# Optimization experiments

Hardware: AMD Instinct MI355X
Metric: run time of the kernel (lower is better)

The kernel has to match this reference:

```python
import jax, jax.numpy as jnp
import numpy as np

CURV = 0.9            # geoopt PoincareBall(0.9)
SQRT_C = CURV ** 0.5
MIN_NORM = 1e-15
PROJ_EPS = 4e-3       # geoopt float32 boundary eps
ATANH_EPS = 1e-7
COS_EPS = 1e-8        # torch.cosine_similarity eps


def _norm(x):
    return jnp.sqrt(jnp.maximum(jnp.sum(x * x, axis=-1, keepdims=True), MIN_NORM * MIN_NORM))


def _project(x):
    # project onto ball of radius (1-eps)/sqrt(c)
    n = jnp.maximum(_norm(x), MIN_NORM)
    maxnorm = (1.0 - PROJ_EPS) / SQRT_C
    return jnp.where(n > maxnorm, x / n * maxnorm, x)


def expmap0(u):
    n = jnp.maximum(_norm(u), MIN_NORM)
    gamma = jnp.tanh(SQRT_C * n) * u / (SQRT_C * n)
    return _project(gamma)


def mobius_add(x, y):
    c = CURV
    x2 = jnp.sum(x * x, axis=-1, keepdims=True)
    y2 = jnp.sum(y * y, axis=-1, keepdims=True)
    xy = jnp.sum(x * y, axis=-1, keepdims=True)
    num = (1.0 + 2.0 * c * xy + c * y2) * x + (1.0 - c * x2) * y
    den = 1.0 + 2.0 * c * xy + c * c * x2 * y2
    return num / jnp.maximum(den, MIN_NORM)


def pdist(x, y):
    # dist(x,y) = 2/sqrt(c) * artanh(sqrt(c) * ||(-x) (+) y||)
    d = mobius_add(-x, y)
    n = _norm(d)[..., 0]
    z = jnp.clip(SQRT_C * n, -1.0 + ATANH_EPS, 1.0 - ATANH_EPS)
    return 2.0 / SQRT_C * jnp.arctanh(z)


def cos_sim(a, b):
    na = jnp.maximum(jnp.sqrt(jnp.sum(a * a, axis=-1)), COS_EPS)
    nb = jnp.maximum(jnp.sqrt(jnp.sum(b * b, axis=-1)), COS_EPS)
    return jnp.sum(a * b, axis=-1) / (na * nb)


def setup_inputs() -> dict:
    key = jax.random.key(0)
    ks = jax.random.split(key, 11)
    B, L, Ls, C, Lc, H, R = 4, 512, 128, 20, 128, 768, 512
    s = 0.02  # keep projected embeddings in a realistic range
    return {
        "text_out": jax.random.normal(ks[0], (B, L, H), jnp.float32),
        "summary_out": jax.random.normal(ks[1], (B, Ls, H), jnp.float32),
        "candidate_out": jax.random.normal(ks[2], (B, C, Lc, H), jnp.float32),
        "W_d": jax.random.normal(ks[3], (H, R), jnp.float32) * s,
        "W_s": jax.random.normal(ks[4], (H, R), jnp.float32) * s,
        "W_c": jax.random.normal(ks[5], (H, R), jnp.float32) * s,
        "W_p": jax.random.normal(ks[6], (R, R), jnp.float32) * s,
        "conv_w1": jax.random.normal(ks[7], (1, H, R), jnp.float32) * s,
        "conv_b1": jax.random.normal(ks[8], (R,), jnp.float32) * s,
        "conv_w2": jax.random.normal(ks[9], (2, H, R), jnp.float32) * s,
        "conv_b2": jax.random.normal(ks[10], (R,), jnp.float32) * s,
    }


def _forward(text_out, summary_out, candidate_out, W_d, W_s, W_c, W_p,
             conv_w1, conv_b1, conv_w2, conv_b2):
    # --- document ---
    doc_emb = expmap0(text_out[:, 0, :] @ W_d)                       # [B,R]

    # NGramers (max_gram=2, eval mode so dropout is identity)
    x = text_out[:, 1:-1, :]                                         # [B,L-2,H]
    y1 = jax.nn.relu(jnp.einsum('blh,hr->blr', x, conv_w1[0]) + conv_b1)
    y2 = jax.nn.relu(jnp.einsum('blh,hr->blr', x[:, :-1], conv_w2[0])
                     + jnp.einsum('blh,hr->blr', x[:, 1:], conv_w2[1]) + conv_b2)
    gram = jnp.concatenate([y1, y2], axis=1)                         # [B,2L-5,R]

    doc_word_emb = expmap0(jnp.einsum('blr,rk->blk', gram, W_p))     # [B,T,R]
    doc_inter = 1.0 / pdist(doc_word_emb, doc_emb[:, None, :])       # [B,T]

    # --- summary ---
    summary_emb = expmap0(jnp.max(summary_out, axis=1) @ W_s)        # [B,R]
    summary_score = -pdist(summary_emb, doc_emb) ** 2                # [B]
    sum_inter = 1.0 / pdist(doc_word_emb, summary_emb[:, None, :])   # [B,T]
    summary_score = summary_score + cos_sim(doc_inter, sum_inter)    # [B]

    # --- candidates ---
    cand_emb = expmap0(jnp.einsum('bch,hr->bcr', jnp.max(candidate_out, axis=2), W_c))  # [B,C,R]
    score = -pdist(cand_emb, doc_emb[:, None, :]) ** 2               # [B,C]
    cand_inter = 1.0 / pdist(doc_word_emb[:, None, :, :], cand_emb[:, :, None, :])      # [B,C,T]
    score = score + cos_sim(doc_inter[:, None, :], cand_inter)       # [B,C]
    return score, summary_score


def reference(text_out, summary_out, candidate_out, W_d, W_s, W_c, W_p,
              conv_w1, conv_b1, conv_w2, conv_b2):
    return _forward(text_out, summary_out, candidate_out, W_d, W_s, W_c, W_p,
                    conv_w1, conv_b1, conv_w2, conv_b2)
```

## Files before the change

### kernel.cpp

```cpp
#include <hip/hip_runtime.h>
#include <math.h>

#define SQRTC  0.94868329805051381f
#define MAXN   (0.996f/SQRTC)
#define OME_CLIP (1.0f - 0.996f*0.996f)
#define TWO_OVER_SQRTC 2.1081851067789197f

typedef unsigned short u16;
typedef __attribute__((ext_vector_type(8))) short bf8;
typedef __attribute__((ext_vector_type(4))) float f4;

__device__ __forceinline__ u16 f2bf(float f){
    union { float f; unsigned int i; } v; v.f = f;
    unsigned int x = v.i;
    unsigned int lsb = (x >> 16) & 1u;
    x += 0x7fffu + lsb;
    return (u16)(x >> 16);
}
__device__ __forceinline__ float bf2f(u16 u){
    union { unsigned int i; float f; } v; v.i = ((unsigned int)u) << 16; return v.f;
}

__device__ __forceinline__ void gload16(void* lds, const void* g){
    __builtin_amdgcn_global_load_lds(
        (const __attribute__((address_space(1))) unsigned int*)g,
        (__attribute__((address_space(3))) unsigned int*)lds,
        16, 0, 0);
}

__device__ __forceinline__ float pdist_stable(float ome_x, float ome_y, float t){
    float u = 1.0f - ome_x, v = 1.0f - ome_y;
    float den = fmaxf(1.0f - 1.8f*t + u*v, 1e-15f);
    float q = ome_x*ome_y/den;
    q = fminf(fmaxf(q, 2.0e-7f), 1.0f);
    float z = sqrtf(fmaxf(1.0f - q, 0.0f));
    float at = 0.5f * logf((1.0f+z)*(1.0f+z)/q);
    return TWO_OVER_SQRTC * at;
}

__device__ __forceinline__ void expmap_scale_ome(float sum, float* fout, float* omeout){
    float nraw = sqrtf(fmaxf(sum, 1e-30f));
    float n = fmaxf(nraw, 1e-15f);
    float sn = SQRTC*n;
    float th = tanhf(sn);
    float factor = th/sn;
    float gn = factor*nraw;
    if (gn > MAXN){ *fout = factor*(MAXN/gn); *omeout = OME_CLIP; }
    else { *fout = factor; *omeout = fmaxf((1.0f-th)*(1.0f+th), 1e-12f); }
}

__global__ __launch_bounds__(256)
void k_stage1(const float* __restrict__ summ, const float* __restrict__ cand,
              const float* __restrict__ text,
              const float* __restrict__ w1, const float* __restrict__ w2,
              const float* __restrict__ wp,
              float* __restrict__ smax, float* __restrict__ cmax,
              u16* __restrict__ textb, u16* __restrict__ w1t,
              u16* __restrict__ w2t, u16* __restrict__ wpt)
{
    __shared__ float shm[1056];
    int bx = blockIdx.x;
    int t = threadIdx.x;
    if (bx < 252){
        int row = bx / 3, hc = bx - row*3;
        int w = t >> 6, lane = t & 63;
        const float* in = (row < 4) ? (summ + (long long)row*128*768)
                                    : (cand + (long long)(row-4)*128*768);
        const float* p = in + (long long)(w*32)*768 + hc*256 + lane*4;
        float4 m = make_float4(-INFINITY,-INFINITY,-INFINITY,-INFINITY);
        #pragma unroll 8
        for (int l = 0; l < 32; l++){
            float4 v = *(const float4*)(p + (long long)l*768);
            m.x = fmaxf(m.x, v.x); m.y = fmaxf(m.y, v.y);
            m.z = fmaxf(m.z, v.z); m.w = fmaxf(m.w, v.w);
        }
        float4* sm4 = (float4*)shm;
        sm4[w*64 + lane] = m; __syncthreads();
        if (t < 64){
            float4 a = sm4[t], b4 = sm4[64+t], c4 = sm4[128+t], d4 = sm4[192+t];
            float4 r;
            r.x = fmaxf(fmaxf(a.x,b4.x), fmaxf(c4.x,d4.x));
            r.y = fmaxf(fmaxf(a.y,b4.y), fmaxf(c4.y,d4.y));
            r.z = fmaxf(fmaxf(a.z,b4.z), fmaxf(c4.z,d4.z));
            r.w = fmaxf(fmaxf(a.w,b4.w), fmaxf(c4.w,d4.w));
            float* outp = (row < 4) ? (smax + row*768) : (cmax + (row-4)*768);
            *(float4*)(outp + hc*256 + t*4) = r;
        }
        return;
    }
    int pb = bx - 252;
    if (pb < 768){
        int base = pb*2048 + t*8;
        float4 a = *(const float4*)(text + base);
        float4 b = *(const float4*)(text + base + 4);
        *(ushort4*)(textb + base)     = make_ushort4(f2bf(a.x), f2bf(a.y), f2bf(a.z), f2bf(a.w));
        *(ushort4*)(textb + base + 4) = make_ushort4(f2bf(b.x), f2bf(b.y), f2bf(b.z), f2bf(b.w));
        return;
    }
    int j = pb - 768;
    const float* in; u16* outp; int K;
    if (j < 384){ in = w1; outp = w1t; K = 768; }
    else if (j < 1152){ j -= 384; in = w2; outp = w2t; K = 1536; }
    else { j -= 1152; in = wp; outp = wpt; K = 512; }
    const int N = 512, ntile = N/32;
    int k0 = (j/ntile)*32, n0 = (j - (j/ntile)*ntile)*32;
    int tx = t & 31, ty = t >> 5;
    #pragma unroll
    for (int i = 0; i < 4; i++)
        shm[(ty*4+i)*33 + tx] = in[(long long)(k0 + ty*4 + i)*N + n0 + tx];
    __syncthreads();
    #pragma unroll
    for (int i = 0; i < 4; i++)
        outp[(long long)(n0 + ty*4 + i)*K + k0 + tx] = f2bf(shm[tx*33 + ty*4+i]);
}

__global__ __launch_bounds__(256)
void k_stage2(const u16* __restrict__ textb,
              const u16* __restrict__ w1t, const u16* __restrict__ w2t,
              const float* __restrict__ cb1, const float* __restrict__ cb2,
              const float* __restrict__ text,
              const float* __restrict__ smax, const float* __restrict__ cmax,
              const float* __restrict__ W_d, const float* __restrict__ W_s,
              const float* __restrict__ W_c,
              u16* __restrict__ gram, float* __restrict__ emb_all)
{
    __shared__ char smem[16384];
    int bx = blockIdx.x;
    int t = threadIdx.x;
    if (bx < 512){
        u16* As = (u16*)smem;
        u16* Bs = (u16*)(smem + 8192);
        int xx = bx & 63, yy = bx >> 6;
        int job = xx & 1;
        int m0 = (xx >> 1) * 64;
        int n0 = yy * 64;
        int K   = job ? 1536 : 768;
        int M   = job ? 2036 : 2040;
        int rpb = job ? 509 : 510;
        int ob  = job ? 510 : 0;
        const u16* Bt = job ? w2t : w1t;
        const float* bias = job ? cb2 : cb1;

        int r0 = t >> 3;
        int co = (((t & 7) ^ (r0 & 7)) << 3);

        int gm0 = m0 + r0;      if (gm0 >= M) gm0 = M - 1;
        int gm1 = m0 + r0 + 32; if (gm1 >= M) gm1 = M - 1;
        int ab0 = gm0 / rpb, al0 = gm0 - ab0*rpb;
        int ab1 = gm1 / rpb, al1 = gm1 - ab1*rpb;
        const u16* a0 = textb + (long long)ab0*393216 + (long long)(al0+1)*768 + co;
        const u16* a1 = textb + (long long)ab1*393216 + (long long)(al1+1)*768 + co;
        const u16* bp0 = Bt + (long long)(n0 + r0)*K      + co;
        const u16* bp1 = Bt + (long long)(n0 + r0 + 32)*K + co;
        u16* lA0 = As + t*8;
        u16* lA1 = As + (256 + t)*8;
        u16* lB0 = Bs + t*8;
        u16* lB1 = Bs + (256 + t)*8;

        int lane = t & 63, wv = t >> 6;
        int fm = lane & 15, fq = lane >> 4;
        int arow = wv*16 + fm;
        int aswz = arow & 7, bswz = fm & 7;
        int aoff0 = arow*64 + ((fq     ^ aswz) << 3);
        int aoff1 = arow*64 + (((4+fq) ^ aswz) << 3);
        int boff0 = ((fq     ^ bswz) << 3);
        int boff1 = (((4+fq) ^ bswz) << 3);

        f4 acc0 = {0,0,0,0}, acc1 = {0,0,0,0}, acc2 = {0,0,0,0}, acc3 = {0,0,0,0};
        for (int k0 = 0; k0 < K; k0 += 64){
            gload16(lA0, a0 + k0);
            gload16(lA1, a1 + k0);
            gload16(lB0, bp0 + k0);
            gload16(lB1, bp1 + k0);
            __syncthreads();
            bf8 af0 = *(const bf8*)(As + aoff0);
            bf8 af1 = *(const bf8*)(As + aoff1);
            bf8 b00 = *(const bf8*)(Bs + (fm   )*64 + boff0);
            bf8 b10 = *(const bf8*)(Bs + (16+fm)*64 + boff0);
            bf8 b20 = *(const bf8*)(Bs + (32+fm)*64 + boff0);
            bf8 b30 = *(const bf8*)(Bs + (48+fm)*64 + boff0);
            bf8 b01 = *(const bf8*)(Bs + (fm   )*64 + boff1);
            bf8 b11 = *(const bf8*)(Bs + (16+fm)*64 + boff1);
            bf8 b21 = *(const bf8*)(Bs + (32+fm)*64 + boff1);
            bf8 b31 = *(const bf8*)(Bs + (48+fm)*64 + boff1);
            acc0 = __builtin_amdgcn_mfma_f32_16x16x32_bf16(af0, b00, acc0, 0, 0, 0);
            acc1 = __builtin_amdgcn_mfma_f32_16x16x32_bf16(af0, b10, acc1, 0, 0, 0);
            acc2 = __builtin_amdgcn_mfma_f32_16x16x32_bf16(af0, b20, acc2, 0, 0, 0);
            acc3 = __builtin_amdgcn_mfma_f32_16x16x32_bf16(af0, b30, acc3, 0, 0, 0);
            acc0 = __builtin_amdgcn_mfma_f32_16x16x32_bf16(af1, b01, acc0, 0, 0, 0);
            acc1 = __builtin_amdgcn_mfma_f32_16x16x32_bf16(af1, b11, acc1, 0, 0, 0);
            acc2 = __builtin_amdgcn_mfma_f32_16x16x32_bf16(af1, b21, acc2, 0, 0, 0);
            acc3 = __builtin_amdgcn_mfma_f32_16x16x32_bf16(af1, b31, acc3, 0, 0, 0);
            __syncthreads();
        }
        int col = n0 + fm;
        float bv0 = bias[col], bv1 = bias[col+16], bv2 = bias[col+32], bv3 = bias[col+48];
        #pragma unroll
        for (int i = 0; i < 4; i++){
            int row = m0 + wv*16 + fq*4 + i;
            if (row >= M) continue;
            int b = row/rpb, l = row - b*rpb;
            long long orow = (long long)b*1019 + ob + l;
            u16* gp = gram + orow*512;
            gp[col]      = f2bf(fmaxf(acc0[i] + bv0, 0.f));
            gp[col + 16] = f2bf(fmaxf(acc1[i] + bv1, 0.f));
            gp[col + 32] = f2bf(fmaxf(acc2[i] + bv2, 0.f));
            gp[col + 48] = f2bf(fmaxf(acc3[i] + bv3, 0.f));
        }
        return;
    }
    {
        int eb = bx - 512;
        int row = eb >> 3, nt = eb & 7;
        float* a   = (float*)smem;
        float* red = (float*)smem + 768;
        const float* A; const float* W;
        if (row < 4){ A = text + (long long)row*512*768; W = W_d; }
        else if (row < 8){ A = smax + (long long)(row-4)*768; W = W_s; }
        else { A = cmax + (long long)(row-8)*768; W = W_c; }
        for (int k = t; k < 768; k += 256) a[k] = A[k];
        __syncthreads();
        int lane = t & 63, kg = t >> 6;
        int col = nt*64 + lane;
        const float* Wp = W + (long long)(kg*192)*512 + col;
        float acc = 0.f;
        #pragma unroll 8
        for (int k = 0; k < 192; k++) acc += a[kg*192 + k] * Wp[k*512];
        red[t] = acc; __syncthreads();
        if (t < 64) emb_all[(long long)row*512 + col] = red[t] + red[t+64] + red[t+128] + red[t+192];
    }
}

__global__ __launch_bounds__(256)
void k_stage3(const u16* __restrict__ gram, const u16* __restrict__ wpt,
              u16* __restrict__ dwe_b,
              float* __restrict__ emb_all, float* __restrict__ ome_all,
              u16* __restrict__ emb_b)
{
    __shared__ char smem[16384];
    int bx = blockIdx.x;
    int t = threadIdx.x;
    if (bx < 512){
        u16* As = (u16*)smem;
        u16* Bs = (u16*)(smem + 8192);
        const int K = 512, M = 4076;
        int m0 = (bx >> 3) * 64;
        int n0 = (bx & 7) * 64;

        int r0 = t >> 3;
        int co = (((t & 7) ^ (r0 & 7)) << 3);
        int gm0 = m0 + r0;      if (gm0 >= M) gm0 = M - 1;
        int gm1 = m0 + r0 + 32; if (gm1 >= M) gm1 = M - 1;
        const u16* a0 = gram + (long long)gm0*512 + co;
        const u16* a1 = gram + (long long)gm1*512 + co;
        const u16* bp0 = wpt + (long long)(n0 + r0)*K      + co;
        const u16* bp1 = wpt + (long long)(n0 + r0 + 32)*K + co;
        u16* lA0 = As + t*8;
        u16* lA1 = As + (256 + t)*8;
        u16* lB0 = Bs + t*8;
        u16* lB1 = Bs + (256 + t)*8;

        int lane = t & 63, wv = t >> 6;
        int fm = lane & 15, fq = lane >> 4;
        int arow = wv*16 + fm;
        int aswz = arow & 7, bswz = fm & 7;
        int aoff0 = arow*64 + ((fq     ^ aswz) << 3);
        int aoff1 = arow*64 + (((4+fq) ^ aswz) << 3);
        int boff0 = ((fq     ^ bswz) << 3);
        int boff1 = (((4+fq) ^ bswz) << 3);

        f4 acc0 = {0,0,0,0}, acc1 = {0,0,0,0}, acc2 = {0,0,0,0}, acc3 = {0,0,0,0};
        for (int k0 = 0; k0 < K; k0 += 64){
            gload16(lA0, a0 + k0);
            gload16(lA1, a1 + k0);
            gload16(lB0, bp0 + k0);
            gload16(lB1, bp1 + k0);
            __syncthreads();
            bf8 af0 = *(const bf8*)(As + aoff0);
            bf8 af1 = *(const bf8*)(As + aoff1);
            bf8 b00 = *(const bf8*)(Bs + (fm   )*64 + boff0);
            bf8 b10 = *(const bf8*)(Bs + (16+fm)*64 + boff0);
            bf8 b20 = *(const bf8*)(Bs + (32+fm)*64 + boff0);
            bf8 b30 = *(const bf8*)(Bs + (48+fm)*64 + boff0);
            bf8 b01 = *(const bf8*)(Bs + (fm   )*64 + boff1);
            bf8 b11 = *(const bf8*)(Bs + (16+fm)*64 + boff1);
            bf8 b21 = *(const bf8*)(Bs + (32+fm)*64 + boff1);
            bf8 b31 = *(const bf8*)(Bs + (48+fm)*64 + boff1);
            acc0 = __builtin_amdgcn_mfma_f32_16x16x32_bf16(af0, b00, acc0, 0, 0, 0);
            acc1 = __builtin_amdgcn_mfma_f32_16x16x32_bf16(af0, b10, acc1, 0, 0, 0);
            acc2 = __builtin_amdgcn_mfma_f32_16x16x32_bf16(af0, b20, acc2, 0, 0, 0);
            acc3 = __builtin_amdgcn_mfma_f32_16x16x32_bf16(af0, b30, acc3, 0, 0, 0);
            acc0 = __builtin_amdgcn_mfma_f32_16x16x32_bf16(af1, b01, acc0, 0, 0, 0);
            acc1 = __builtin_amdgcn_mfma_f32_16x16x32_bf16(af1, b11, acc1, 0, 0, 0);
            acc2 = __builtin_amdgcn_mfma_f32_16x16x32_bf16(af1, b21, acc2, 0, 0, 0);
            acc3 = __builtin_amdgcn_mfma_f32_16x16x32_bf16(af1, b31, acc3, 0, 0, 0);
            __syncthreads();
        }
        int col = n0 + fm;
        #pragma unroll
        for (int i = 0; i < 4; i++){
            int row = m0 + wv*16 + fq*4 + i;
            if (row >= M) continue;
            u16* dp = dwe_b + (long long)row*512;
            dp[col]      = f2bf(acc0[i]);
            dp[col + 16] = f2bf(acc1[i]);
            dp[col + 32] = f2bf(acc2[i]);
            dp[col + 48] = f2bf(acc3[i]);
        }
        return;
    }
    {
        float* red = (float*)smem;
        int row = bx - 512;
        float* X = emb_all + (long long)row*512;
        float2 u = *(float2*)(X + t*2);
        red[t] = u.x*u.x + u.y*u.y; __syncthreads();
        for (int s = 128; s > 0; s >>= 1){ if (t < s) red[t] += red[t+s]; __syncthreads(); }
        float f, ome;
        expmap_scale_ome(red[0], &f, &ome);
        float sx = u.x*f, sy = u.y*f;
        *(float2*)(X + t*2) = make_float2(sx, sy);
        u16* Xb = emb_b + (long long)row*512;
        Xb[t*2]   = f2bf(sx);
        Xb[t*2+1] = f2bf(sy);
        if (t == 0) ome_all[row] = ome;
    }
}

__global__ __launch_bounds__(64)
void k_dots_mfma(const u16* __restrict__ dwe_b, const u16* __restrict__ emb_b,
                 const float* __restrict__ ome_all,
                 float* __restrict__ doc_inter, float* __restrict__ sum_inter,
                 float* __restrict__ cand_inter)
{
    int bx = blockIdx.x;
    int b  = bx >> 6;
    int m0 = (bx & 63) * 16;
    int t = threadIdx.x;
    int fm = t & 15, fq = t >> 4;

    int arow = m0 + fm; if (arow > 1018) arow = 1018;
    const u16* Ap = dwe_b + ((long long)(b*1019 + arow))*512 + fq*8;

    int n1 = 16 + fm; if (n1 > 21) n1 = 21;
    int e0 = (fm == 0) ? b : (fm == 1) ? 4 + b : 8 + b*20 + (fm - 2);
    int e1 = 8 + b*20 + (n1 - 2);
    const u16* B0 = emb_b + (long long)e0*512 + fq*8;
    const u16* B1 = emb_b + (long long)e1*512 + fq*8;
    float oy0 = ome_all[e0];
    float oy1 = ome_all[e1];

    f4 acc0 = {0,0,0,0}, acc1 = {0,0,0,0};
    float ssq = 0.f;
    #pragma unroll 4
    for (int k0 = 0; k0 < 512; k0 += 32){
        bf8 av  = *(const bf8*)(Ap + k0);
        bf8 bv0 = *(const bf8*)(B0 + k0);
        bf8 bv1 = *(const bf8*)(B1 + k0);
        #pragma unroll
        for (int j = 0; j < 8; j++){ float x = bf2f(((u16*)&av)[j]); ssq += x*x; }
        acc0 = __builtin_amdgcn_mfma_f32_16x16x32_bf16(av, bv0, acc0, 0, 0, 0);
        acc1 = __builtin_amdgcn_mfma_f32_16x16x32_bf16(av, bv1, acc1, 0, 0, 0);
    }
    ssq += __shfl_xor(ssq, 16);
    ssq += __shfl_xor(ssq, 32);

    #pragma unroll
    for (int i = 0; i < 4; i++){
        int r = fq*4 + i;
        float rs = __shfl(ssq, r);
        int row = m0 + r;
        if (row >= 1019) continue;
        float f, ox;
        expmap_scale_ome(rs, &f, &ox);
        long long grow = (long long)b*1019 + row;
        {
            float s = acc0[i] * f;
            float dist = pdist_stable(ox, oy0, s);
            float inv = 1.0f/fmaxf(dist, 1e-12f);
            if (fm == 0) doc_inter[grow] = inv;
            else if (fm == 1) sum_inter[grow] = inv;
            else cand_inter[((long long)(b*20 + (fm - 2)))*1019 + row] = inv;
        }
        if (16 + fm < 22){
            float s = acc1[i] * f;
            float dist = pdist_stable(ox, oy1, s);
            float inv = 1.0f/fmaxf(dist, 1e-12f);
            cand_inter[((long long)(b*20 + (16 + fm - 2)))*1019 + row] = inv;
        }
    }
}

__global__ __launch_bounds__(256)
void k_final(const float* __restrict__ doc_inter, const float* __restrict__ sum_inter,
             const float* __restrict__ cand_inter,
             const float* __restrict__ emb_all, const float* __restrict__ ome_all,
             float* __restrict__ out)
{
    __shared__ float r0[256], r1[256], r2[256], r3[256];
    int j = blockIdx.x, t = threadIdx.x;
    int b; const float *a, *bb; int xi, yi; int outIdx;
    if (j < 80){
        b = j/20;
        a  = doc_inter + b*1019;
        bb = cand_inter + (long long)j*1019;
        xi = 8 + j; yi = b;
        outIdx = j;
    } else {
        b = j - 80;
        a  = doc_inter + b*1019;
        bb = sum_inter + b*1019;
        xi = 4 + b; yi = b;
        outIdx = 80 + b;
    }
    const float* xe = emb_all + (long long)xi*512;
    const float* ye = emb_all + (long long)yi*512;
    float ox = ome_all[xi], oy = ome_all[yi];
    float saa = 0.f, sbb = 0.f, sab = 0.f, st = 0.f;
    for (int l = t; l < 1019; l += 256){ float av = a[l], bv = bb[l]; saa += av*av; sbb += bv*bv; sab += av*bv; }
    for (int k = t; k < 512; k += 256) st += xe[k]*ye[k];
    r0[t] = saa; r1[t] = sbb; r2[t] = sab; r3[t] = st; __syncthreads();
    for (int s = 128; s > 0; s >>= 1){
        if (t < s){ r0[t] += r0[t+s]; r1[t] += r1[t+s]; r2[t] += r2[t+s]; r3[t] += r3[t+s]; }
        __syncthreads();
    }
    if (t == 0){
        float na = fmaxf(sqrtf(r0[0]), 1e-8f);
        float nb = fmaxf(sqrtf(r1[0]), 1e-8f);
        float cosv = r2[0] / (na*nb);
        float pd = pdist_stable(ox, oy, r3[0]);
        out[outIdx] = -pd*pd + cosv;
    }
}

extern "C" void kernel_launch(void* const* d_in, const int* in_sizes, int n_in,
                              void* d_out, int out_size, void* d_ws, size_t ws_size,
                              hipStream_t stream) {
    const float* text = (const float*)d_in[0];
    const float* summ = (const float*)d_in[1];
    const float* cand = (const float*)d_in[2];
    const float* W_d  = (const float*)d_in[3];
    const float* W_s  = (const float*)d_in[4];
    const float* W_c  = (const float*)d_in[5];
    const float* W_p  = (const float*)d_in[6];
    const float* cw1  = (const float*)d_in[7];
    const float* cb1  = (const float*)d_in[8];
    const float* cw2  = (const float*)d_in[9];
    const float* cb2  = (const float*)d_in[10];
    float* out = (float*)d_out;

    const int B = 4, C = 20, H = 768;

    char* base = (char*)d_ws;
    size_t off = 0;
    auto allocF = [&](size_t n)->float*{ float* p = (float*)(base + off); off += ((n*4) + 255) & ~(size_t)255; return p; };
    auto allocU = [&](size_t n)->u16*{ u16* p = (u16*)(base + off); off += ((n*2) + 255) & ~(size_t)255; return p; };

    float* smax = allocF(B*H);
    float* cmax = allocF(B*C*H);
    float* emb_all = allocF(88*512);
    float* ome_all = allocF(88);
    u16* emb_b = allocU(88*512);
    u16* textb = allocU(4*512*768);
    u16* w1t   = allocU(512*768);
    u16* w2t   = allocU(512*1536);
    u16* wpt   = allocU(512*512);
    u16* gram  = allocU(4076*512);
    u16* dwe_b = allocU(4076*512);
    float* doc_inter = allocF(4076);
    float* sum_inter = allocF(4076);
    float* cand_inter= allocF(B*C*1019);

    k_stage1<<<2428, 256, 0, stream>>>(summ, cand, text, cw1, cw2, W_p,
                                       smax, cmax, textb, w1t, w2t, wpt);

    k_stage2<<<1216, 256, 0, stream>>>(textb, w1t, w2t, cb1, cb2,
                                       text, smax, cmax, W_d, W_s, W_c,
                                       gram, emb_all);

    k_stage3<<<600, 256, 0, stream>>>(gram, wpt, dwe_b, emb_all, ome_all, emb_b);

    k_dots_mfma<<<256, 64, 0, stream>>>(dwe_b, emb_b, ome_all,
                                        doc_inter, sum_inter, cand_inter);

    k_final<<<84, 256, 0, stream>>>(doc_inter, sum_inter, cand_inter,
                                    emb_all, ome_all, out);
}
```

Measured before the change: 141.4 us.

## Double-buffer LDS tiles in stage2 and stage3 GEMMs to overlap loads with MFMA

Both bf16 MFMA GEMM paths now use two LDS buffers for A and B. The global-to-LDS loads for the next K tile are issued before computing the current one, with explicit vmcnt waits and raw s_barrier in place of __syncthreads. The aim is to hide global load latency behind the MFMA work. The cost is doubled shared memory per block, which may reduce occupancy. Correctness now depends on the hand-written waitcnt and barrier ordering.

```diff
diff --git a/kernel.cpp b/kernel.cpp
--- a/kernel.cpp
+++ b/kernel.cpp
@@ -124,12 +124,14 @@
               const float* __restrict__ W_c,
               u16* __restrict__ gram, float* __restrict__ emb_all)
 {
-    __shared__ char smem[16384];
+    __shared__ char smem[32768];
     int bx = blockIdx.x;
     int t = threadIdx.x;
     if (bx < 512){
-        u16* As = (u16*)smem;
-        u16* Bs = (u16*)(smem + 8192);
+        u16* As0 = (u16*)smem;
+        u16* Bs0 = (u16*)(smem + 8192);
+        u16* As1 = (u16*)(smem + 16384);
+        u16* Bs1 = (u16*)(smem + 24576);
         int xx = bx & 63, yy = bx >> 6;
         int job = xx & 1;
         int m0 = (xx >> 1) * 64;
@@ -152,10 +154,7 @@
         const u16* a1 = textb + (long long)ab1*393216 + (long long)(al1+1)*768 + co;
         const u16* bp0 = Bt + (long long)(n0 + r0)*K      + co;
         const u16* bp1 = Bt + (long long)(n0 + r0 + 32)*K + co;
-        u16* lA0 = As + t*8;
-        u16* lA1 = As + (256 + t)*8;
-        u16* lB0 = Bs + t*8;
-        u16* lB1 = Bs + (256 + t)*8;
+        int d0 = t*8, d1 = (256 + t)*8;
 
         int lane = t & 63, wv = t >> 6;
         int fm = lane & 15, fq = lane >> 4;
@@ -167,22 +166,37 @@
         int boff1 = (((4+fq) ^ bswz) << 3);
 
         f4 acc0 = {0,0,0,0}, acc1 = {0,0,0,0}, acc2 = {0,0,0,0}, acc3 = {0,0,0,0};
-        for (int k0 = 0; k0 < K; k0 += 64){
-            gload16(lA0, a0 + k0);
-            gload16(lA1, a1 + k0);
-            gload16(lB0, bp0 + k0);
-            gload16(lB1, bp1 + k0);
-            __syncthreads();
-            bf8 af0 = *(const bf8*)(As + aoff0);
-            bf8 af1 = *(const bf8*)(As + aoff1);
-            bf8 b00 = *(const bf8*)(Bs + (fm   )*64 + boff0);
-            bf8 b10 = *(const bf8*)(Bs + (16+fm)*64 + boff0);
-            bf8 b20 = *(const bf8*)(Bs + (32+fm)*64 + boff0);
-            bf8 b30 = *(const bf8*)(Bs + (48+fm)*64 + boff0);
-            bf8 b01 = *(const bf8*)(Bs + (fm   )*64 + boff1);
-            bf8 b11 = *(const bf8*)(Bs + (16+fm)*64 + boff1);
-            bf8 b21 = *(const bf8*)(Bs + (32+fm)*64 + boff1);
-            bf8 b31 = *(const bf8*)(Bs + (48+fm)*64 + boff1);
+        const int nt = K >> 6;
+        gload16(As0 + d0, a0);
+        gload16(As0 + d1, a1);
+        gload16(Bs0 + d0, bp0);
+        gload16(Bs0 + d1, bp1);
+        for (int i = 0; i < nt; i++){
+            u16* Ac = (i & 1) ? As1 : As0;
+            u16* Bc = (i & 1) ? Bs1 : Bs0;
+            if (i + 1 < nt){
+                u16* An = (i & 1) ? As0 : As1;
+                u16* Bn = (i & 1) ? Bs0 : Bs1;
+                int kn = (i + 1) << 6;
+                gload16(An + d0, a0 + kn);
+                gload16(An + d1, a1 + kn);
+                gload16(Bn + d0, bp0 + kn);
+                gload16(Bn + d1, bp1 + kn);
+                asm volatile("s_waitcnt vmcnt(4)" ::: "memory");
+            } else {
+                asm volatile("s_waitcnt vmcnt(0)" ::: "memory");
+            }
+            __builtin_amdgcn_s_barrier();
+            bf8 af0 = *(const bf8*)(Ac + aoff0);
+            bf8 af1 = *(const bf8*)(Ac + aoff1);
+            bf8 b00 = *(const bf8*)(Bc + (fm   )*64 + boff0);
+            bf8 b10 = *(const bf8*)(Bc + (16+fm)*64 + boff0);
+            bf8 b20 = *(const bf8*)(Bc + (32+fm)*64 + boff0);
+            bf8 b30 = *(const bf8*)(Bc + (48+fm)*64 + boff0);
+            bf8 b01 = *(const bf8*)(Bc + (fm   )*64 + boff1);
+            bf8 b11 = *(const bf8*)(Bc + (16+fm)*64 + boff1);
+            bf8 b21 = *(const bf8*)(Bc + (32+fm)*64 + boff1);
+            bf8 b31 = *(const bf8*)(Bc + (48+fm)*64 + boff1);
             acc0 = __builtin_amdgcn_mfma_f32_16x16x32_bf16(af0, b00, acc0, 0, 0, 0);
             acc1 = __builtin_amdgcn_mfma_f32_16x16x32_bf16(af0, b10, acc1, 0, 0, 0);
             acc2 = __builtin_amdgcn_mfma_f32_16x16x32_bf16(af0, b20, acc2, 0, 0, 0);
@@ -191,7 +205,7 @@
             acc1 = __builtin_amdgcn_mfma_f32_16x16x32_bf16(af1, b11, acc1, 0, 0, 0);
             acc2 = __builtin_amdgcn_mfma_f32_16x16x32_bf16(af1, b21, acc2, 0, 0, 0);
             acc3 = __builtin_amdgcn_mfma_f32_16x16x32_bf16(af1, b31, acc3, 0, 0, 0);
-            __syncthreads();
+            __builtin_amdgcn_s_barrier();
         }
         int col = n0 + fm;
         float bv0 = bias[col], bv1 = bias[col+16], bv2 = bias[col+32], bv3 = bias[col+48];
@@ -237,12 +251,14 @@
               float* __restrict__ emb_all, float* __restrict__ ome_all,
               u16* __restrict__ emb_b)
 {
-    __shared__ char smem[16384];
+    __shared__ char smem[32768];
     int bx = blockIdx.x;
     int t = threadIdx.x;
     if (bx < 512){
-        u16* As = (u16*)smem;
-        u16* Bs = (u16*)(smem + 8192);
+        u16* As0 = (u16*)smem;
+        u16* Bs0 = (u16*)(smem + 8192);
+        u16* As1 = (u16*)(smem + 16384);
+        u16* Bs1 = (u16*)(smem + 24576);
         const int K = 512, M = 4076;
         int m0 = (bx >> 3) * 64;
         int n0 = (bx & 7) * 64;
@@ -255,10 +271,7 @@
         const u16* a1 = gram + (long long)gm1*512 + co;
         const u16* bp0 = wpt + (long long)(n0 + r0)*K      + co;
         const u16* bp1 = wpt + (long long)(n0 + r0 + 32)*K + co;
-        u16* lA0 = As + t*8;
-        u16* lA1 = As + (256 + t)*8;
-        u16* lB0 = Bs + t*8;
-        u16* lB1 = Bs + (256 + t)*8;
+        int d0 = t*8, d1 = (256 + t)*8;
 
         int lane = t & 63, wv = t >> 6;
         int fm = lane & 15, fq = lane >> 4;
@@ -270,22 +283,37 @@
         int boff1 = (((4+fq) ^ bswz) << 3);
 
         f4 acc0 = {0,0,0,0}, acc1 = {0,0,0,0}, acc2 = {0,0,0,0}, acc3 = {0,0,0,0};
-        for (int k0 = 0; k0 < K; k0 += 64){
-            gload16(lA0, a0 + k0);
-            gload16(lA1, a1 + k0);
-            gload16(lB0, bp0 + k0);
-            gload16(lB1, bp1 + k0);
-            __syncthreads();
-            bf8 af0 = *(const bf8*)(As + aoff0);
-            bf8 af1 = *(const bf8*)(As + aoff1);
-            bf8 b00 = *(const bf8*)(Bs + (fm   )*64 + boff0);
-            bf8 b10 = *(const bf8*)(Bs + (16+fm)*64 + boff0);
-            bf8 b20 = *(const bf8*)(Bs + (32+fm)*64 + boff0);
-            bf8 b30 = *(const bf8*)(Bs + (48+fm)*64 + boff0);
-            bf8 b01 = *(const bf8*)(Bs + (fm   )*64 + boff1);
-            bf8 b11 = *(const bf8*)(Bs + (16+fm)*64 + boff1);
-            bf8 b21 = *(const bf8*)(Bs + (32+fm)*64 + boff1);
-            bf8 b31 = *(const bf8*)(Bs + (48+fm)*64 + boff1);
+        const int nt = K >> 6;
+        gload16(As0 + d0, a0);
+        gload16(As0 + d1, a1);
+        gload16(Bs0 + d0, bp0);
+        gload16(Bs0 + d1, bp1);
+        for (int i = 0; i < nt; i++){
+            u16* Ac = (i & 1) ? As1 : As0;
+            u16* Bc = (i & 1) ? Bs1 : Bs0;
+            if (i + 1 < nt){
+                u16* An = (i & 1) ? As0 : As1;
+                u16* Bn = (i & 1) ? Bs0 : Bs1;
+                int kn = (i + 1) << 6;
+                gload16(An + d0, a0 + kn);
+                gload16(An + d1, a1 + kn);
+                gload16(Bn + d0, bp0 + kn);
+                gload16(Bn + d1, bp1 + kn);
+                asm volatile("s_waitcnt vmcnt(4)" ::: "memory");
+            } else {
+                asm volatile("s_waitcnt vmcnt(0)" ::: "memory");
+            }
+            __builtin_amdgcn_s_barrier();
+            bf8 af0 = *(const bf8*)(Ac + aoff0);
+            bf8 af1 = *(const bf8*)(Ac + aoff1);
+            bf8 b00 = *(const bf8*)(Bc + (fm   )*64 + boff0);
+            bf8 b10 = *(const bf8*)(Bc + (16+fm)*64 + boff0);
+            bf8 b20 = *(const bf8*)(Bc + (32+fm)*64 + boff0);
+            bf8 b30 = *(const bf8*)(Bc + (48+fm)*64 + boff0);
+            bf8 b01 = *(const bf8*)(Bc + (fm   )*64 + boff1);
+            bf8 b11 = *(const bf8*)(Bc + (16+fm)*64 + boff1);
+            bf8 b21 = *(const bf8*)(Bc + (32+fm)*64 + boff1);
+            bf8 b31 = *(const bf8*)(Bc + (48+fm)*64 + boff1);
             acc0 = __builtin_amdgcn_mfma_f32_16x16x32_bf16(af0, b00, acc0, 0, 0, 0);
             acc1 = __builtin_amdgcn_mfma_f32_16x16x32_bf16(af0, b10, acc1, 0, 0, 0);
             acc2 = __builtin_amdgcn_mfma_f32_16x16x32_bf16(af0, b20, acc2, 0, 0, 0);
@@ -294,7 +322,7 @@
             acc1 = __builtin_amdgcn_mfma_f32_16x16x32_bf16(af1, b11, acc1, 0, 0, 0);
             acc2 = __builtin_amdgcn_mfma_f32_16x16x32_bf16(af1, b21, acc2, 0, 0, 0);
             acc3 = __builtin_amdgcn_mfma_f32_16x16x32_bf16(af1, b31, acc3, 0, 0, 0);
-            __syncthreads();
+            __builtin_amdgcn_s_barrier();
         }
         int col = n0 + fm;
         #pragma unroll
```

Result: no change. 139.9 us, median of 2 (-1.0%).
